# Performance work log

Hardware: AMD Instinct MI355X
Metric: run time of the kernel (lower is better)

The kernel has to match this reference:

```python
import jax, jax.numpy as jnp
import numpy as np

N_NODES = 50000


def gcn_conv(x, W, b, src, dst, n_nodes):
    """PyG GCNConv: x' = D^-1/2 (A+I) D^-1/2 (x W) + b (symmetric norm, self-loops)."""
    h = x @ W  # [N, out]
    loop = jnp.arange(n_nodes, dtype=src.dtype)
    src_f = jnp.concatenate([src, loop])
    dst_f = jnp.concatenate([dst, loop])
    ones = jnp.ones(src_f.shape[0], dtype=h.dtype)
    deg = jax.ops.segment_sum(ones, dst_f, num_segments=n_nodes)
    dinv = jnp.where(deg > 0, jax.lax.rsqrt(deg), 0.0)
    norm = dinv[src_f] * dinv[dst_f]  # [E+N]
    msg = h[src_f] * norm[:, None]    # irregular gather over edges
    out = jax.ops.segment_sum(msg, dst_f, num_segments=n_nodes)
    return out + b


def setup_inputs() -> dict:
    key = jax.random.key(0)
    ks = jax.random.split(key, 9)
    d_in, d_h = 128, 128
    x = jax.random.normal(ks[0], (N_NODES, d_in), dtype=jnp.float32)
    edge_index = jax.random.randint(ks[1], (2, 800000), 0, N_NODES, dtype=jnp.int64)
    glorot = lambda k, fi, fo: jax.random.normal(k, (fi, fo), dtype=jnp.float32) * jnp.sqrt(2.0 / (fi + fo))
    return {
        "x": x,
        "edge_index": edge_index,
        "W1": glorot(ks[2], d_in, d_h), "b1": jnp.zeros((d_h,), jnp.float32),
        "W2": glorot(ks[3], d_h, d_h), "b2": jnp.zeros((d_h,), jnp.float32),
        "W3": glorot(ks[4], d_h, d_h), "b3": jnp.zeros((d_h,), jnp.float32),
    }


def reference(x, edge_index, W1, b1, W2, b2, W3, b3):
    src, dst = edge_index[0], edge_index[1]
    n = x.shape[0]
    h = jax.nn.relu(gcn_conv(x, W1, b1, src, dst, n))
    h = jax.nn.relu(gcn_conv(h, W2, b2, src, dst, n))
    h = gcn_conv(h, W3, b3, src, dst, n)
    return h
```

## Files before the change

kernel.cpp:

```cpp
#include <hip/hip_runtime.h>

#define N_NODES 50000
#define N_EDGES 800000
#define DIM 128
#define MAXDEG 64
#define EDGE_BLOCKS ((N_EDGES + 255) / 256)
#define WT_BLOCKS 192
#define GEMM_BLOCKS ((N_NODES + 127) / 128)

typedef unsigned int u32;
typedef short bf16x8 __attribute__((ext_vector_type(8)));
typedef float f32x4 __attribute__((ext_vector_type(4)));

static inline size_t alignUp(size_t x) { return (x + 255) & ~size_t(255); }

__device__ inline unsigned short f2bf(float f) {
    union { float f; u32 u; } v; v.f = f;
    u32 r = v.u + 0x7fffu + ((v.u >> 16) & 1u);
    return (unsigned short)(r >> 16);
}
__device__ inline float bf_lo(u32 u) { return __uint_as_float(u << 16); }
__device__ inline float bf_hi(u32 u) { return __uint_as_float(u & 0xffff0000u); }

__global__ __launch_bounds__(256) void prep_kernel(const float* __restrict__ W1,
                                                   const float* __restrict__ W2,
                                                   const float* __restrict__ W3,
                                                   unsigned short* __restrict__ Wt,
                                                   const int* __restrict__ src,
                                                   const int* __restrict__ dst,
                                                   int* __restrict__ cursor,
                                                   int* __restrict__ csr_dm) {
    int bid = blockIdx.x;
    if (bid < WT_BLOCKS) {
        int m = bid >> 6;
        int e = (bid & 63) * 256 + threadIdx.x;
        int n = e >> 7, k = e & 127;
        const float* W = (m == 0) ? W1 : (m == 1) ? W2 : W3;
        Wt[m * DIM * DIM + n * DIM + k] = f2bf(W[(size_t)k * DIM + n]);
        return;
    }
    int i = (bid - WT_BLOCKS) * 256 + threadIdx.x;
    if (i < N_EDGES) {
        int d = dst[i];
        int pos = atomicAdd(&cursor[d], 1);
        if (pos < MAXDEG) csr_dm[d * MAXDEG + pos] = src[i];
    }
}

__global__ __launch_bounds__(256) void pack_kernel(const int* __restrict__ cnt,
                                                   const int* __restrict__ csr_dm,
                                                   int2* __restrict__ epk) {
    int wave = threadIdx.x >> 6;
    int lane = threadIdx.x & 63;
    int node = blockIdx.x * 4 + wave;
    if (node >= N_NODES) return;
    int m = min(cnt[node], MAXDEG);
    if (lane < m) {
        int s = csr_dm[node * MAXDEG + lane];
        float w = rsqrtf((float)(cnt[s] + 1));
        epk[node * MAXDEG + lane] = make_int2(s, __float_as_int(w));
    }
}

#define LDSTRIDE 40
__device__ void gemm_core(unsigned short* As, unsigned short* Bs,
                          const unsigned short* __restrict__ Wt,
                          unsigned short* __restrict__ hb, int n_rows, int row0,
                          bool stage_f32, const float* xf, const unsigned short* xb) {
    const int tid = threadIdx.x;
    const int wave = tid >> 6;
    const int lane = tid & 63;
    const int quad = lane >> 4;
    const int l16 = lane & 15;

    f32x4 acc[2][8];
#pragma unroll
    for (int mt = 0; mt < 2; mt++)
#pragma unroll
        for (int nt = 0; nt < 8; nt++) acc[mt][nt] = (f32x4){0.f, 0.f, 0.f, 0.f};

    for (int k0 = 0; k0 < DIM; k0 += 32) {
        if (stage_f32) {
#pragma unroll
            for (int p = 0; p < 4; p++) {
                int r = p * 32 + (tid >> 3);
                int kq = (tid & 7) * 4;
                int gr = row0 + r;
                float4 v = make_float4(0.f, 0.f, 0.f, 0.f);
                if (gr < n_rows) v = *(const float4*)&xf[(size_t)gr * DIM + k0 + kq];
                u32 lo = (u32)f2bf(v.x) | ((u32)f2bf(v.y) << 16);
                u32 hi = (u32)f2bf(v.z) | ((u32)f2bf(v.w) << 16);
                *(uint2*)&As[r * LDSTRIDE + kq] = make_uint2(lo, hi);
            }
        } else {
#pragma unroll
            for (int p = 0; p < 2; p++) {
                int idx = p * 256 + tid;
                int r = idx >> 2;
                int c = idx & 3;
                int gr = row0 + r;
                uint4 v = make_uint4(0, 0, 0, 0);
                if (gr < n_rows) v = *(const uint4*)&xb[(size_t)gr * DIM + k0 + c * 8];
                *(uint4*)&As[r * LDSTRIDE + c * 8] = v;
            }
        }
#pragma unroll
        for (int p = 0; p < 2; p++) {
            int nn = p * 64 + (tid >> 2);
            int kk = (tid & 3) * 8;
            *(uint4*)&Bs[nn * LDSTRIDE + kk] = *(const uint4*)&Wt[nn * DIM + k0 + kk];
        }
        __syncthreads();
        const int m0 = wave * 32;
        bf16x8 a0 = *(const bf16x8*)&As[(m0 + l16) * LDSTRIDE + quad * 8];
        bf16x8 a1 = *(const bf16x8*)&As[(m0 + 16 + l16) * LDSTRIDE + quad * 8];
#pragma unroll
        for (int nt = 0; nt < 8; nt++) {
            bf16x8 b = *(const bf16x8*)&Bs[(nt * 16 + l16) * LDSTRIDE + quad * 8];
            acc[0][nt] = __builtin_amdgcn_mfma_f32_16x16x32_bf16(a0, b, acc[0][nt], 0, 0, 0);
            acc[1][nt] = __builtin_amdgcn_mfma_f32_16x16x32_bf16(a1, b, acc[1][nt], 0, 0, 0);
        }
        __syncthreads();
    }
    const int m0 = wave * 32;
#pragma unroll
    for (int mt = 0; mt < 2; mt++) {
#pragma unroll
        for (int reg = 0; reg < 4; reg++) {
            int gr = row0 + m0 + mt * 16 + quad * 4 + reg;
            if (gr < n_rows) {
#pragma unroll
                for (int nt = 0; nt < 8; nt++)
                    hb[(size_t)gr * DIM + nt * 16 + l16] = f2bf(acc[mt][nt][reg]);
            }
        }
    }
}

__global__ __launch_bounds__(256) void gemm_f32_kernel(const float* __restrict__ x,
                                                       const unsigned short* __restrict__ Wt,
                                                       unsigned short* __restrict__ hb, int n) {
    __shared__ unsigned short As[128 * LDSTRIDE];
    __shared__ unsigned short Bs[128 * LDSTRIDE];
    gemm_core(As, Bs, Wt, hb, n, blockIdx.x * 128, true, x, nullptr);
}

__global__ __launch_bounds__(256) void gemm_bf16_kernel(const unsigned short* __restrict__ x,
                                                        const unsigned short* __restrict__ Wt,
                                                        unsigned short* __restrict__ hb, int n) {
    __shared__ unsigned short As[128 * LDSTRIDE];
    __shared__ unsigned short Bs[128 * LDSTRIDE];
    gemm_core(As, Bs, Wt, hb, n, blockIdx.x * 128, false, nullptr, x);
}

__device__ inline void accum8(float acc[8], uint4 r, float w) {
    acc[0] += w * bf_lo(r.x); acc[1] += w * bf_hi(r.x);
    acc[2] += w * bf_lo(r.y); acc[3] += w * bf_hi(r.y);
    acc[4] += w * bf_lo(r.z); acc[5] += w * bf_hi(r.z);
    acc[6] += w * bf_lo(r.w); acc[7] += w * bf_hi(r.w);
}

__global__ __launch_bounds__(256) void agg_kernel(const uint4* __restrict__ hb,
                                                  const int* __restrict__ cnt,
                                                  const int2* __restrict__ epk,
                                                  const float4* __restrict__ bias4,
                                                  unsigned short* __restrict__ out_bf,
                                                  float* __restrict__ out_f32,
                                                  int relu_bf16) {
    const int wave = threadIdx.x >> 6;
    const int lane = threadIdx.x & 63;
    const int node = blockIdx.x * 4 + wave;
    const int g = lane >> 4;
    const int l16 = lane & 15;

    const int deg = cnt[node];
    const float di = rsqrtf((float)(deg + 1));
    const int m = min(deg, MAXDEG);
    const int2* base = epk + node * MAXDEG;

    float acc[8];
#pragma unroll
    for (int i = 0; i < 8; i++) acc[i] = 0.f;

    for (int j0 = 0; j0 < m; j0 += 16) {
        int jA = j0 + g, jB = j0 + 4 + g, jC = j0 + 8 + g, jD = j0 + 12 + g;
        int2 pA = base[min(jA, m - 1)];
        int2 pB = base[min(jB, m - 1)];
        int2 pC = base[min(jC, m - 1)];
        int2 pD = base[min(jD, m - 1)];
        uint4 rA = hb[(size_t)pA.x * 16 + l16];
        uint4 rB = hb[(size_t)pB.x * 16 + l16];
        uint4 rC = hb[(size_t)pC.x * 16 + l16];
        uint4 rD = hb[(size_t)pD.x * 16 + l16];
        float wA = (jA < m) ? __int_as_float(pA.y) : 0.f;
        float wB = (jB < m) ? __int_as_float(pB.y) : 0.f;
        float wC = (jC < m) ? __int_as_float(pC.y) : 0.f;
        float wD = (jD < m) ? __int_as_float(pD.y) : 0.f;
        accum8(acc, rA, wA);
        accum8(acc, rB, wB);
        accum8(acc, rC, wC);
        accum8(acc, rD, wD);
    }
    if (g == 0) {
        uint4 r = hb[(size_t)node * 16 + l16];
        accum8(acc, r, di);
    }
#pragma unroll
    for (int i = 0; i < 8; i++) {
        acc[i] += __shfl_xor(acc[i], 16, 64);
        acc[i] += __shfl_xor(acc[i], 32, 64);
    }
    if (g == 0) {
        float4 b0 = bias4[l16 * 2], b1 = bias4[l16 * 2 + 1];
        float v[8];
        v[0] = di * acc[0] + b0.x; v[1] = di * acc[1] + b0.y;
        v[2] = di * acc[2] + b0.z; v[3] = di * acc[3] + b0.w;
        v[4] = di * acc[4] + b1.x; v[5] = di * acc[5] + b1.y;
        v[6] = di * acc[6] + b1.z; v[7] = di * acc[7] + b1.w;
        if (relu_bf16) {
            uint4 pk;
            u32* p = (u32*)&pk;
#pragma unroll
            for (int i = 0; i < 4; i++) {
                float a = fmaxf(v[2 * i], 0.f), b = fmaxf(v[2 * i + 1], 0.f);
                p[i] = (u32)f2bf(a) | ((u32)f2bf(b) << 16);
            }
            ((uint4*)(out_bf + (size_t)node * DIM))[l16] = pk;
        } else {
            float4* o = (float4*)(out_f32 + (size_t)node * DIM);
            o[l16 * 2] = make_float4(v[0], v[1], v[2], v[3]);
            o[l16 * 2 + 1] = make_float4(v[4], v[5], v[6], v[7]);
        }
    }
}


extern "C" void kernel_launch(void* const* d_in, const int* in_sizes, int n_in,
                              void* d_out, int out_size, void* d_ws, size_t ws_size,
                              hipStream_t stream) {
    const float* x  = (const float*)d_in[0];
    const int* ei   = (const int*)d_in[1];
    const float* W1 = (const float*)d_in[2];
    const float* b1 = (const float*)d_in[3];
    const float* W2 = (const float*)d_in[4];
    const float* b2 = (const float*)d_in[5];
    const float* W3 = (const float*)d_in[6];
    const float* b3 = (const float*)d_in[7];
    const int* src = ei;
    const int* dst = ei + N_EDGES;
    float* out = (float*)d_out;

    char* w = (char*)d_ws;
    int* cursor = (int*)w; w += alignUp((size_t)N_NODES * 4);
    int* csr_dm = (int*)w; w += alignUp((size_t)N_NODES * MAXDEG * 4);
    int2* epk   = (int2*)w; w += alignUp((size_t)N_NODES * MAXDEG * 8);
    unsigned short* wt = (unsigned short*)w; w += alignUp((size_t)3 * DIM * DIM * 2);
    unsigned short* hbuf = (unsigned short*)w; w += alignUp((size_t)N_NODES * DIM * 2);
    unsigned short* gbuf = (unsigned short*)w; w += alignUp((size_t)N_NODES * DIM * 2);

    hipMemsetAsync(cursor, 0, (size_t)N_NODES * 4, stream);

    prep_kernel<<<WT_BLOCKS + EDGE_BLOCKS, 256, 0, stream>>>(W1, W2, W3, wt, src, dst,
                                                             cursor, csr_dm);
    pack_kernel<<<(N_NODES + 3) / 4, 256, 0, stream>>>(cursor, csr_dm, epk);

    int ablocks = (N_NODES + 3) / 4;

    gemm_f32_kernel<<<GEMM_BLOCKS, 256, 0, stream>>>(x, wt, hbuf, N_NODES);
    agg_kernel<<<ablocks, 256, 0, stream>>>((const uint4*)hbuf, cursor, epk,
                                            (const float4*)b1, gbuf, nullptr, 1);

    gemm_bf16_kernel<<<GEMM_BLOCKS, 256, 0, stream>>>(gbuf, wt + DIM * DIM, hbuf, N_NODES);
    agg_kernel<<<ablocks, 256, 0, stream>>>((const uint4*)hbuf, cursor, epk,
                                            (const float4*)b2, gbuf, nullptr, 1);

    gemm_bf16_kernel<<<GEMM_BLOCKS, 256, 0, stream>>>(gbuf, wt + 2 * DIM * DIM, hbuf, N_NODES);
    agg_kernel<<<ablocks, 256, 0, stream>>>((const uint4*)hbuf, cursor, epk,
                                            (const float4*)b3, nullptr, out, 0);
}
```

Before: 282.3 us.

## Fold source-side degree norm into GEMM epilogue and pad CSR with zero row

Result: slower. 302.9 us (+7.3%).

```diff
diff --git a/kernel.cpp b/kernel.cpp
--- a/kernel.cpp
+++ b/kernel.cpp
@@ -7,6 +7,7 @@
 #define EDGE_BLOCKS ((N_EDGES + 255) / 256)
 #define WT_BLOCKS 192
 #define GEMM_BLOCKS ((N_NODES + 127) / 128)
+#define ZERO_ROW N_NODES
 
 typedef unsigned int u32;
 typedef short bf16x8 __attribute__((ext_vector_type(8)));
@@ -47,24 +48,25 @@
     }
 }
 
-__global__ __launch_bounds__(256) void pack_kernel(const int* __restrict__ cnt,
-                                                   const int* __restrict__ csr_dm,
-                                                   int2* __restrict__ epk) {
+__global__ __launch_bounds__(256) void finalize_kernel(const int* __restrict__ cnt,
+                                                       int* __restrict__ csr_dm,
+                                                       float* __restrict__ dinv) {
     int wave = threadIdx.x >> 6;
     int lane = threadIdx.x & 63;
     int node = blockIdx.x * 4 + wave;
     if (node >= N_NODES) return;
-    int m = min(cnt[node], MAXDEG);
-    if (lane < m) {
-        int s = csr_dm[node * MAXDEG + lane];
-        float w = rsqrtf((float)(cnt[s] + 1));
-        epk[node * MAXDEG + lane] = make_int2(s, __float_as_int(w));
-    }
+    int c = cnt[node];
+    int m = min(c, MAXDEG);
+    int m_pad = (m + 15) & ~15;
+    if (lane == 0) dinv[node] = rsqrtf((float)(c + 1));
+    int j = m + lane;
+    if (j < m_pad) csr_dm[node * MAXDEG + j] = ZERO_ROW;
 }
 
 #define LDSTRIDE 40
 __device__ void gemm_core(unsigned short* As, unsigned short* Bs,
                           const unsigned short* __restrict__ Wt,
+                          const float* __restrict__ dinv,
                           unsigned short* __restrict__ hb, int n_rows, int row0,
                           bool stage_f32, const float* xf, const unsigned short* xb) {
     const int tid = threadIdx.x;
@@ -129,9 +131,10 @@
         for (int reg = 0; reg < 4; reg++) {
             int gr = row0 + m0 + mt * 16 + quad * 4 + reg;
             if (gr < n_rows) {
+                float dv = dinv[gr];
 #pragma unroll
                 for (int nt = 0; nt < 8; nt++)
-                    hb[(size_t)gr * DIM + nt * 16 + l16] = f2bf(acc[mt][nt][reg]);
+                    hb[(size_t)gr * DIM + nt * 16 + l16] = f2bf(dv * acc[mt][nt][reg]);
             }
         }
     }
@@ -139,30 +142,32 @@
 
 __global__ __launch_bounds__(256) void gemm_f32_kernel(const float* __restrict__ x,
                                                        const unsigned short* __restrict__ Wt,
+                                                       const float* __restrict__ dinv,
                                                        unsigned short* __restrict__ hb, int n) {
     __shared__ unsigned short As[128 * LDSTRIDE];
     __shared__ unsigned short Bs[128 * LDSTRIDE];
-    gemm_core(As, Bs, Wt, hb, n, blockIdx.x * 128, true, x, nullptr);
+    gemm_core(As, Bs, Wt, dinv, hb, n, blockIdx.x * 128, true, x, nullptr);
 }
 
 __global__ __launch_bounds__(256) void gemm_bf16_kernel(const unsigned short* __restrict__ x,
                                                         const unsigned short* __restrict__ Wt,
+                                                        const float* __restrict__ dinv,
                                                         unsigned short* __restrict__ hb, int n) {
     __shared__ unsigned short As[128 * LDSTRIDE];
     __shared__ unsigned short Bs[128 * LDSTRIDE];
-    gemm_core(As, Bs, Wt, hb, n, blockIdx.x * 128, false, nullptr, x);
-}
-
-__device__ inline void accum8(float acc[8], uint4 r, float w) {
-    acc[0] += w * bf_lo(r.x); acc[1] += w * bf_hi(r.x);
-    acc[2] += w * bf_lo(r.y); acc[3] += w * bf_hi(r.y);
-    acc[4] += w * bf_lo(r.z); acc[5] += w * bf_hi(r.z);
-    acc[6] += w * bf_lo(r.w); acc[7] += w * bf_hi(r.w);
+    gemm_core(As, Bs, Wt, dinv, hb, n, blockIdx.x * 128, false, nullptr, x);
+}
+
+__device__ inline void add8(float acc[8], uint4 r) {
+    acc[0] += bf_lo(r.x); acc[1] += bf_hi(r.x);
+    acc[2] += bf_lo(r.y); acc[3] += bf_hi(r.y);
+    acc[4] += bf_lo(r.z); acc[5] += bf_hi(r.z);
+    acc[6] += bf_lo(r.w); acc[7] += bf_hi(r.w);
 }
 
 __global__ __launch_bounds__(256) void agg_kernel(const uint4* __restrict__ hb,
                                                   const int* __restrict__ cnt,
-                                                  const int2* __restrict__ epk,
+                                                  const int* __restrict__ csr,
                                                   const float4* __restrict__ bias4,
                                                   unsigned short* __restrict__ out_bf,
                                                   float* __restrict__ out_f32,
@@ -173,37 +178,33 @@
     const int g = lane >> 4;
     const int l16 = lane & 15;
 
-    const int deg = cnt[node];
-    const float di = rsqrtf((float)(deg + 1));
-    const int m = min(deg, MAXDEG);
-    const int2* base = epk + node * MAXDEG;
+    const int c = cnt[node];
+    const float di = rsqrtf((float)(c + 1));
+    const int m = min(c, MAXDEG);
+    const int m_pad = (m + 15) & ~15;
+    const int* cp = csr + node * MAXDEG;
 
     float acc[8];
 #pragma unroll
     for (int i = 0; i < 8; i++) acc[i] = 0.f;
 
-    for (int j0 = 0; j0 < m; j0 += 16) {
-        int jA = j0 + g, jB = j0 + 4 + g, jC = j0 + 8 + g, jD = j0 + 12 + g;
-        int2 pA = base[min(jA, m - 1)];
-        int2 pB = base[min(jB, m - 1)];
-        int2 pC = base[min(jC, m - 1)];
-        int2 pD = base[min(jD, m - 1)];
-        uint4 rA = hb[(size_t)pA.x * 16 + l16];
-        uint4 rB = hb[(size_t)pB.x * 16 + l16];
-        uint4 rC = hb[(size_t)pC.x * 16 + l16];
-        uint4 rD = hb[(size_t)pD.x * 16 + l16];
-        float wA = (jA < m) ? __int_as_float(pA.y) : 0.f;
-        float wB = (jB < m) ? __int_as_float(pB.y) : 0.f;
-        float wC = (jC < m) ? __int_as_float(pC.y) : 0.f;
-        float wD = (jD < m) ? __int_as_float(pD.y) : 0.f;
-        accum8(acc, rA, wA);
-        accum8(acc, rB, wB);
-        accum8(acc, rC, wC);
-        accum8(acc, rD, wD);
+    for (int j0 = 0; j0 < m_pad; j0 += 16) {
+        int sA = cp[j0 + g];
+        int sB = cp[j0 + 4 + g];
+        int sC = cp[j0 + 8 + g];
+        int sD = cp[j0 + 12 + g];
+        uint4 rA = hb[(size_t)sA * 16 + l16];
+        uint4 rB = hb[(size_t)sB * 16 + l16];
+        uint4 rC = hb[(size_t)sC * 16 + l16];
+        uint4 rD = hb[(size_t)sD * 16 + l16];
+        add8(acc, rA);
+        add8(acc, rB);
+        add8(acc, rC);
+        add8(acc, rD);
     }
     if (g == 0) {
         uint4 r = hb[(size_t)node * 16 + l16];
-        accum8(acc, r, di);
+        add8(acc, r);
     }
 #pragma unroll
     for (int i = 0; i < 8; i++) {
@@ -253,28 +254,29 @@
     char* w = (char*)d_ws;
     int* cursor = (int*)w; w += alignUp((size_t)N_NODES * 4);
     int* csr_dm = (int*)w; w += alignUp((size_t)N_NODES * MAXDEG * 4);
-    int2* epk   = (int2*)w; w += alignUp((size_t)N_NODES * MAXDEG * 8);
+    float* dinv = (float*)w; w += alignUp((size_t)N_NODES * 4);
     unsigned short* wt = (unsigned short*)w; w += alignUp((size_t)3 * DIM * DIM * 2);
-    unsigned short* hbuf = (unsigned short*)w; w += alignUp((size_t)N_NODES * DIM * 2);
+    unsigned short* hbuf = (unsigned short*)w; w += alignUp((size_t)(N_NODES + 1) * DIM * 2);
     unsigned short* gbuf = (unsigned short*)w; w += alignUp((size_t)N_NODES * DIM * 2);
 
     hipMemsetAsync(cursor, 0, (size_t)N_NODES * 4, stream);
+    hipMemsetAsync(hbuf + (size_t)ZERO_ROW * DIM, 0, DIM * 2, stream);
 
     prep_kernel<<<WT_BLOCKS + EDGE_BLOCKS, 256, 0, stream>>>(W1, W2, W3, wt, src, dst,
                                                              cursor, csr_dm);
-    pack_kernel<<<(N_NODES + 3) / 4, 256, 0, stream>>>(cursor, csr_dm, epk);
+    finalize_kernel<<<(N_NODES + 3) / 4, 256, 0, stream>>>(cursor, csr_dm, dinv);
 
     int ablocks = (N_NODES + 3) / 4;
 
-    gemm_f32_kernel<<<GEMM_BLOCKS, 256, 0, stream>>>(x, wt, hbuf, N_NODES);
-    agg_kernel<<<ablocks, 256, 0, stream>>>((const uint4*)hbuf, cursor, epk,
+    gemm_f32_kernel<<<GEMM_BLOCKS, 256, 0, stream>>>(x, wt, dinv, hbuf, N_NODES);
+    agg_kernel<<<ablocks, 256, 0, stream>>>((const uint4*)hbuf, cursor, csr_dm,
                                             (const float4*)b1, gbuf, nullptr, 1);
 
-    gemm_bf16_kernel<<<GEMM_BLOCKS, 256, 0, stream>>>(gbuf, wt + DIM * DIM, hbuf, N_NODES);
-    agg_kernel<<<ablocks, 256, 0, stream>>>((const uint4*)hbuf, cursor, epk,
+    gemm_bf16_kernel<<<GEMM_BLOCKS, 256, 0, stream>>>(gbuf, wt + DIM * DIM, dinv, hbuf, N_NODES);
+    agg_kernel<<<ablocks, 256, 0, stream>>>((const uint4*)hbuf, cursor, csr_dm,
                                             (const float4*)b2, gbuf, nullptr, 1);
 
-    gemm_bf16_kernel<<<GEMM_BLOCKS, 256, 0, stream>>>(gbuf, wt + 2 * DIM * DIM, hbuf, N_NODES);
-    agg_kernel<<<ablocks, 256, 0, stream>>>((const uint4*)hbuf, cursor, epk,
+    gemm_bf16_kernel<<<GEMM_BLOCKS, 256, 0, stream>>>(gbuf, wt + 2 * DIM * DIM, dinv, hbuf, N_NODES);
+    agg_kernel<<<ablocks, 256, 0, stream>>>((const uint4*)hbuf, cursor, csr_dm,
                                             (const float4*)b3, nullptr, out, 0);
 }
```
